# Optimization experiments

Hardware: AMD Instinct MI355X
Metric: run time of the kernel (lower is better)

Reference implementation:

```python
import jax, jax.numpy as jnp
import numpy as np

B, N, IN_CH = 4, 8192, 4
K = 16
W0, W1, W2 = 64, 128, 256
NUM_CLASSES = 3


def setup_inputs() -> dict:
    key = jax.random.key(0)
    ks = jax.random.split(key, 16)

    def lin(kw, kb, fan_in, fan_out):
        bound = 1.0 / np.sqrt(fan_in)
        w = jax.random.uniform(kw, (fan_in, fan_out), jnp.float32, -bound, bound)
        b = jax.random.uniform(kb, (fan_out,), jnp.float32, -bound, bound)
        return w, b

    x = jax.random.normal(ks[0], (B, N, IN_CH), jnp.float32)
    stem_w, stem_b = lin(ks[1], ks[2], IN_CH, W0)
    b1_w, b1_b = lin(ks[3], ks[4], 2 * W0 + 3, W1)
    b2_w, b2_b = lin(ks[5], ks[6], 2 * W1 + 3, W2)
    glob_w, glob_b = lin(ks[7], ks[8], W2, W2)
    head1_w, head1_b = lin(ks[9], ks[10], 2 * W2, W2)
    head2_w, head2_b = lin(ks[11], ks[12], W2, NUM_CLASSES)
    return {
        'x': x,
        'hmix_a': jnp.float32(1.0), 'hmix_b': jnp.float32(1.0), 'hmix_c': jnp.float32(0.0),
        'stem_w': stem_w, 'stem_b': stem_b,
        'b1_w': b1_w, 'b1_b': b1_b,
        'b2_w': b2_w, 'b2_b': b2_b,
        'glob_w': glob_w, 'glob_b': glob_b,
        'head1_w': head1_w, 'head1_b': head1_b,
        'head2_w': head2_w, 'head2_b': head2_b,
        'thresh': jnp.float32(0.15), 'sharp': jnp.float32(10.0), 'scale': jnp.float32(0.5),
    }


def _knn_idx(coords, k):
    # coords: [B,N,3] -> idx of k nearest neighbors (incl. self), no grad.
    c = jax.lax.stop_gradient(coords)
    xx = jnp.sum(c * c, axis=-1, keepdims=True)            # [B,N,1]
    dist = xx + jnp.swapaxes(xx, 1, 2) - 2.0 * jnp.einsum('bnc,bmc->bnm', c, c)
    dist = jnp.maximum(dist, 0.0)
    _, idx = jax.lax.top_k(-dist, k)                       # smallest distances
    return idx                                             # [B,N,k]


def _local_agg(coords, feat, idx, w, b):
    # gather-concat-MLP-maxpool, faithful to LocalAggBlock (pool='max')
    bidx = jnp.arange(coords.shape[0])[:, None, None]
    nb_f = feat[bidx, idx]                                 # [B,N,k,C]
    nb_p = coords[bidx, idx]                               # [B,N,k,3]
    fi = feat[:, :, None, :]
    pi = coords[:, :, None, :]
    h = jnp.concatenate(
        [jnp.broadcast_to(fi, nb_f.shape), nb_f - fi, nb_p - pi], axis=-1)
    h = jax.nn.relu(jnp.einsum('bnkd,do->bnko', h, w) + b)
    return jnp.max(h, axis=2)                              # [B,N,out]


def reference(x, hmix_a, hmix_b, hmix_c, stem_w, stem_b, b1_w, b1_b,
              b2_w, b2_b, glob_w, glob_b, head1_w, head1_b,
              head2_w, head2_b, thresh, sharp, scale):
    # HeightMixer: z_eff = a*z + b*hag + c
    z_eff = hmix_a * x[..., 2] + hmix_b * x[..., 3] + hmix_c
    coords = jnp.stack([x[..., 0], x[..., 1], z_eff], axis=-1)  # [B,N,3]

    f = jax.nn.relu(x @ stem_w + stem_b)                   # stem: [B,N,64]

    # both blocks use the same coords -> same KNN graph; compute once
    idx = _knn_idx(coords, K)
    f = _local_agg(coords, f, idx, b1_w, b1_b)             # [B,N,128]
    f = _local_agg(coords, f, idx, b2_w, b2_b)             # [B,N,256]

    g = jnp.max(f, axis=1)                                 # [B,256]
    g = jax.nn.relu(g @ glob_w + glob_b)
    g = jnp.broadcast_to(g[:, None, :], f.shape)           # [B,N,256]

    h = jnp.concatenate([f, g], axis=-1)                   # [B,N,512]
    h = jax.nn.relu(h @ head1_w + head1_b)
    logits = h @ head2_w + head2_b                         # [B,N,3]

    # HeightPriorBias on class 0
    hag = x[..., 3]
    bias = scale * jax.nn.sigmoid(sharp * (thresh - hag))
    logits = logits.at[..., 0].add(bias)
    return logits
```

## Files before the change

kernel.cpp:

```cpp
#include <hip/hip_runtime.h>
#include <math.h>

typedef unsigned long long u64;
typedef unsigned int u32;
typedef _Float16 h8v __attribute__((ext_vector_type(8)));
typedef float    f4v __attribute__((ext_vector_type(4)));
typedef float    f2v __attribute__((ext_vector_type(2)));

#define MFMA16(a,b,c) __builtin_amdgcn_mfma_f32_16x16x32_f16(a, b, c, 0, 0, 0)

#define B_ 4
#define N_ 8192
#define K_ 16
#define W0_ 64
#define W1_ 128
#define W2_ 256
#define X0_ 96
#define X1_ 160

__global__ __launch_bounds__(256) void prep_kernel(
    const float* __restrict__ x,
    const float* __restrict__ stem_w, const float* __restrict__ stem_b,
    const float* __restrict__ hmix_a, const float* __restrict__ hmix_b,
    const float* __restrict__ hmix_c,
    float* __restrict__ coords4, _Float16* __restrict__ fx0,
    _Float16* __restrict__ fx1,
    const float* __restrict__ b1_w, const float* __restrict__ b2_w,
    const float* __restrict__ h1w,
    _Float16* __restrict__ w1m, _Float16* __restrict__ w1d,
    _Float16* __restrict__ w2m, _Float16* __restrict__ w2d,
    _Float16* __restrict__ h1wT) {
  const int bi = blockIdx.x;
  const int tid = threadIdx.x;
  const int PB = (B_*N_)/4;
  if (bi < PB) {
    const int p = bi * 4 + (tid >> 6);
    const int o = tid & 63;
    const float x0 = x[p*4+0], x1 = x[p*4+1], x2 = x[p*4+2], x3 = x[p*4+3];
    const float z = hmix_a[0]*x2 + hmix_b[0]*x3 + hmix_c[0];
    float acc = stem_b[o] + x0*stem_w[0*W0_+o] + x1*stem_w[1*W0_+o]
              + x2*stem_w[2*W0_+o] + x3*stem_w[3*W0_+o];
    fx0[p*X0_+o] = (_Float16)fmaxf(acc, 0.f);
    if (o < 32) {
      const float tv = (o==0) ? x0 : (o==1) ? x1 : (o==2) ? z : 0.f;
      fx0[p*X0_+W0_+o] = (_Float16)tv;
      fx1[(size_t)p*X1_+W1_+o] = (_Float16)tv;
    }
    if (o == 0) {
      const float xx = x0*x0 + x1*x1 + z*z;
      ((float4*)coords4)[p] = make_float4(x0, x1, z, xx);
    }
  } else if (bi < PB + W1_) {
    const int o = bi - PB, c = tid;
    if (c < X0_) {
      float mv = 0.f, dv = 0.f;
      if (c < W0_)        { const float wm = b1_w[(W0_+c)*W1_+o]; mv = wm; dv = b1_w[c*W1_+o] - wm; }
      else if (c < W0_+3) { const float wp = b1_w[(2*W0_+(c-W0_))*W1_+o]; mv = wp; dv = -wp; }
      w1m[o*X0_+c] = (_Float16)mv;
      w1d[o*X0_+c] = (_Float16)dv;
    }
  } else if (bi < PB + W1_ + W2_) {
    const int o = bi - PB - W1_, c = tid;
    if (c < X1_) {
      float mv = 0.f, dv = 0.f;
      if (c < W1_)        { const float wm = b2_w[(W1_+c)*W2_+o]; mv = wm; dv = b2_w[c*W2_+o] - wm; }
      else if (c < W1_+3) { const float wp = b2_w[(2*W1_+(c-W1_))*W2_+o]; mv = wp; dv = -wp; }
      w2m[o*X1_+c] = (_Float16)mv;
      w2d[o*X1_+c] = (_Float16)dv;
    }
  } else {
    const int o = bi - PB - W1_ - W2_;
    for (int c = tid; c < 512; c += 256)
      h1wT[(size_t)o*512 + c] = (_Float16)h1w[(size_t)c*256 + o];
  }
}

#define DPP_SHR1(v) __builtin_amdgcn_update_dpp(0, (v), 0x138, 0xF, 0xF, false)

#define DPP_MIN(v, ctrl)                                                        \
  { const int _t = __builtin_amdgcn_update_dpp(__float_as_int(v),               \
      __float_as_int(v), ctrl, 0xF, 0xF, false);                                \
    v = fminf(v, __int_as_float(_t)); }

__device__ __forceinline__ float sixteenth_of_minima(float v) {
  float th = 0.f;
#pragma unroll
  for (int r = 0; r < 16; ++r) {
    float w = v;
    DPP_MIN(w, 0x111); DPP_MIN(w, 0x112); DPP_MIN(w, 0x114); DPP_MIN(w, 0x118);
    DPP_MIN(w, 0x142); DPP_MIN(w, 0x143);
    const float mv = __int_as_float(
        __builtin_amdgcn_readlane(__float_as_int(w), 63));
    th = mv;
    v = (v == mv) ? INFINITY : v;
  }
  return th;
}

#define KNN_EVT(d, dk, ik)                                                      \
  {                                                                             \
    const int s = (int)__ffsll((unsigned long long)m) - 1;  m &= m - 1;         \
    const float dc = __int_as_float(__builtin_amdgcn_readlane(                  \
                       __float_as_int(d), s));                                  \
    const bool cnd = dc < dk;                                                   \
    const u64 cm = __ballot(cnd) << 1;                                          \
    const float pd = __int_as_float(DPP_SHR1(__float_as_int(dk)));              \
    const int   pi = DPP_SHR1(ik);                                              \
    const bool pc = (cm >> lane) & 1;                                           \
    dk = cnd ? (pc ? pd : dc) : dk;                                             \
    ik = cnd ? (pc ? pi : (jbase + s)) : ik;                                    \
  }

#define KNN_CHUNK(d, dk, ik, T, Th)                                             \
  { u64 m = __ballot(d <= T);                                                   \
    if (m) {                                                                    \
      do { KNN_EVT(d, dk, ik) } while (m);                                      \
      T = fminf(Th, __int_as_float(__builtin_amdgcn_readlane(                   \
            __float_as_int(dk), 15)));                                          \
    }                                                                           \
  }

#define KNN_DIST2(dA, dB)                                                       \
  const f2v cjx = {cj.x, cj.x}, cjy = {cj.y, cj.y},                             \
            cjz = {cj.z, cj.z}, cjw = {cj.w, cj.w};                             \
  f2v tA = cAx * cjx;                                                           \
  tA = __builtin_elementwise_fma(cAy, cjy, tA);                                 \
  tA = __builtin_elementwise_fma(cAz, cjz, tA);                                 \
  const f2v dA = __builtin_elementwise_fma(tA, m2, cAw + cjw);                  \
  f2v tB = cBx * cjx;                                                           \
  tB = __builtin_elementwise_fma(cBy, cjy, tB);                                 \
  tB = __builtin_elementwise_fma(cBz, cjz, tB);                                 \
  const f2v dB = __builtin_elementwise_fma(tB, m2, cBw + cjw);

__global__ __launch_bounds__(256, 8) void knn_kernel(
    const float* __restrict__ coords4, int* __restrict__ knn_idx) {
  const int tid = threadIdx.x;
  const int wid = tid >> 6;
  const int lane = tid & 63;
  const int p0 = blockIdx.x * 16 + wid * 4;
  const int b = p0 >> 13;
  const float4* cb = ((const float4*)coords4) + (b << 13);
  const float4 c0 = ((const float4*)coords4)[p0+0];
  const float4 c1 = ((const float4*)coords4)[p0+1];
  const float4 c2 = ((const float4*)coords4)[p0+2];
  const float4 c3 = ((const float4*)coords4)[p0+3];
  const f2v m2 = {-2.f, -2.f};
  const f2v cAx = {c0.x, c1.x}, cAy = {c0.y, c1.y}, cAz = {c0.z, c1.z}, cAw = {c0.w, c1.w};
  const f2v cBx = {c2.x, c3.x}, cBy = {c2.y, c3.y}, cBz = {c2.z, c3.z}, cBw = {c2.w, c3.w};

  float lm0 = INFINITY, lm1 = INFINITY, lm2 = INFINITY, lm3 = INFINITY;
  for (int it = 0; it < 64; ++it) {
    const float4 cj = cb[it*64 + lane];
    KNN_DIST2(dA, dB)
    lm0 = fminf(lm0, fmaxf(dA[0], 0.f));
    lm1 = fminf(lm1, fmaxf(dA[1], 0.f));
    lm2 = fminf(lm2, fmaxf(dB[0], 0.f));
    lm3 = fminf(lm3, fmaxf(dB[1], 0.f));
  }
  const float Th0 = sixteenth_of_minima(lm0);
  const float Th1 = sixteenth_of_minima(lm1);
  const float Th2 = sixteenth_of_minima(lm2);
  const float Th3 = sixteenth_of_minima(lm3);

  float dk0 = INFINITY, dk1 = INFINITY, dk2 = INFINITY, dk3 = INFINITY;
  int   ik0 = 0, ik1 = 0, ik2 = 0, ik3 = 0;
  float T0 = Th0, T1 = Th1, T2 = Th2, T3 = Th3;

  for (int it = 0; it < N_/64; ++it) {
    const int jbase = it*64;
    const float4 cj = cb[jbase + lane];
    KNN_DIST2(dA, dB)
    const float d0 = fmaxf(dA[0], 0.f);
    const float d1 = fmaxf(dA[1], 0.f);
    const float d2 = fmaxf(dB[0], 0.f);
    const float d3 = fmaxf(dB[1], 0.f);
    KNN_CHUNK(d0, dk0, ik0, T0, Th0);
    KNN_CHUNK(d1, dk1, ik1, T1, Th1);
    KNN_CHUNK(d2, dk2, ik2, T2, Th2);
    KNN_CHUNK(d3, dk3, ik3, T3, Th3);
  }

  if (lane < K_) {
    knn_idx[(size_t)(p0+0)*K_ + lane] = ik0;
    knn_idx[(size_t)(p0+1)*K_ + lane] = ik1;
    knn_idx[(size_t)(p0+2)*K_ + lane] = ik2;
    knn_idx[(size_t)(p0+3)*K_ + lane] = ik3;
  }
}

template<int KS, int NPASS, bool GMAX>
__global__ __launch_bounds__(256) void aggm_kernel(
    const _Float16* __restrict__ fx, const int* __restrict__ knn_idx,
    const _Float16* __restrict__ midT, const _Float16* __restrict__ difT,
    const float* __restrict__ bw,
    _Float16* __restrict__ fo, const int ostr, u32* __restrict__ part) {
  const int XD  = KS*32;
  const int XDP = XD + 8;
  const int CH  = KS*4;
  const int p0 = blockIdx.x * 16;
  const int bb = (p0 >> 13) << 13;
  const int tid = threadIdx.x;
  const int w = tid >> 6, lane = tid & 63, col = lane & 15, quad = lane >> 4;
  const int koff = quad * 8;

  __shared__ int s_idx[256];
  __shared__ _Float16 sA[2][16*(KS*32+8)];

  s_idx[tid] = knn_idx[p0*K_ + tid];

  f4v cacc[NPASS][2];
  {
    h8v Ao[KS];
    const _Float16* ap = fx + (size_t)(p0+col)*XD + koff;
#pragma unroll
    for (int kk = 0; kk < KS; ++kk) Ao[kk] = *(const h8v*)(ap + kk*32);
#pragma unroll
    for (int ps = 0; ps < NPASS; ++ps) {
      const int o0 = ps*128 + w*32;
      const _Float16* b0 = difT + (size_t)(o0 + col)*XD + koff;
      const _Float16* b1 = difT + (size_t)(o0 + 16 + col)*XD + koff;
      f4v c0 = {0.f,0.f,0.f,0.f}, c1 = {0.f,0.f,0.f,0.f};
#pragma unroll
      for (int kk = 0; kk < KS; ++kk) {
        c0 = MFMA16(Ao[kk], *(const h8v*)(b0 + kk*32), c0);
        c1 = MFMA16(Ao[kk], *(const h8v*)(b1 + kk*32), c1);
      }
      cacc[ps][0] = c0; cacc[ps][1] = c1;
    }
  }

  h8v Bf[NPASS][2][KS];
  float bias[NPASS][2];
#pragma unroll
  for (int ps = 0; ps < NPASS; ++ps) {
    const int o0 = ps*128 + w*32;
#pragma unroll
    for (int kk = 0; kk < KS; ++kk) {
      Bf[ps][0][kk] = *(const h8v*)(midT + (size_t)(o0 + col)*XD + kk*32 + koff);
      Bf[ps][1][kk] = *(const h8v*)(midT + (size_t)(o0 + 16 + col)*XD + kk*32 + koff);
    }
    bias[ps][0] = bw[o0 + col];
    bias[ps][1] = bw[o0 + 16 + col];
  }
  __syncthreads();

  for (int c = tid; c < 16*CH; c += 256) {
    const int r = c / CH, o = c - r*CH;
    *(uint4*)&sA[0][r*XDP + o*8] =
        *(const uint4*)(fx + (size_t)(bb + s_idx[r<<4])*XD + o*8);
  }
  __syncthreads();

  f4v M[NPASS][2];
#pragma unroll
  for (int ps = 0; ps < NPASS; ++ps) {
    M[ps][0] = (f4v){-INFINITY,-INFINITY,-INFINITY,-INFINITY};
    M[ps][1] = (f4v){-INFINITY,-INFINITY,-INFINITY,-INFINITY};
  }

  for (int k = 0; k < 16; ++k) {
    const int buf = k & 1;
    if (k < 15) {
      for (int c = tid; c < 16*CH; c += 256) {
        const int r = c / CH, o = c - r*CH;
        *(uint4*)&sA[buf^1][r*XDP + o*8] =
            *(const uint4*)(fx + (size_t)(bb + s_idx[(r<<4) + k + 1])*XD + o*8);
      }
    }
    h8v Ac[KS];
    const _Float16* ap = &sA[buf][col*XDP + koff];
#pragma unroll
    for (int kk = 0; kk < KS; ++kk) Ac[kk] = *(const h8v*)(ap + kk*32);
#pragma unroll
    for (int ps = 0; ps < NPASS; ++ps) {
      f4v d0 = {0.f,0.f,0.f,0.f}, d1 = {0.f,0.f,0.f,0.f};
#pragma unroll
      for (int kk = 0; kk < KS; ++kk) {
        d0 = MFMA16(Ac[kk], Bf[ps][0][kk], d0);
        d1 = MFMA16(Ac[kk], Bf[ps][1][kk], d1);
      }
#pragma unroll
      for (int e = 0; e < 4; ++e) {
        M[ps][0][e] = fmaxf(M[ps][0][e], d0[e]);
        M[ps][1][e] = fmaxf(M[ps][1][e], d1[e]);
      }
    }
    __syncthreads();
  }

  const int prow = p0 + (quad << 2);
  const int bq = p0 >> 13;
#pragma unroll
  for (int ps = 0; ps < NPASS; ++ps) {
    const int o0 = ps*128 + w*32;
    const int oa = o0 + col, ob = oa + 16;
    float v0[4], v1[4];
#pragma unroll
    for (int reg = 0; reg < 4; ++reg) {
      v0[reg] = fmaxf(M[ps][0][reg] + cacc[ps][0][reg] + bias[ps][0], 0.f);
      v1[reg] = fmaxf(M[ps][1][reg] + cacc[ps][1][reg] + bias[ps][1], 0.f);
      fo[(size_t)(prow+reg)*ostr + oa] = (_Float16)v0[reg];
      fo[(size_t)(prow+reg)*ostr + ob] = (_Float16)v1[reg];
    }
    if (GMAX) {
      float bm0 = fmaxf(fmaxf(v0[0], v0[1]), fmaxf(v0[2], v0[3]));
      float bm1 = fmaxf(fmaxf(v1[0], v1[1]), fmaxf(v1[2], v1[3]));
      bm0 = fmaxf(bm0, __shfl_xor(bm0, 16, 64));
      bm0 = fmaxf(bm0, __shfl_xor(bm0, 32, 64));
      bm1 = fmaxf(bm1, __shfl_xor(bm1, 16, 64));
      bm1 = fmaxf(bm1, __shfl_xor(bm1, 32, 64));
      if (quad == 0) {
        atomicMax(part + bq*W2_ + oa, __float_as_uint(bm0));
        atomicMax(part + bq*W2_ + ob, __float_as_uint(bm1));
      }
    }
  }
}

__global__ __launch_bounds__(256) void gfc_kernel(
    const float* __restrict__ part, const float* __restrict__ gw,
    const float* __restrict__ gb, _Float16* __restrict__ g2h) {
  const int b = blockIdx.x;
  const int o = threadIdx.x;
  __shared__ float s_g[W2_];
  s_g[o] = part[b*W2_ + o];
  __syncthreads();
  float acc = gb[o];
  for (int d = 0; d < W2_; ++d) acc += s_g[d]*gw[d*W2_ + o];
  g2h[b*W2_ + o] = (_Float16)fmaxf(acc, 0.f);
}

__global__ __launch_bounds__(256) void headm_kernel(
    const _Float16* __restrict__ f2h, const _Float16* __restrict__ g2h,
    const _Float16* __restrict__ h1wT, const float* __restrict__ h1b,
    const float* __restrict__ h2w, const float* __restrict__ h2b,
    const float* __restrict__ x,
    const float* __restrict__ thresh, const float* __restrict__ sharp,
    const float* __restrict__ scale,
    float* __restrict__ out) {
  const int p0 = blockIdx.x * 32;
  const int b = p0 >> 13;
  const int tid = threadIdx.x;
  const int w = tid >> 6, lane = tid & 63, col = lane & 15, quad = lane >> 4;

  __shared__ _Float16 sA[32*520];
  __shared__ float    sh[32*260];

  for (int t = tid; t < 32*32; t += 256) {
    const int r = t >> 5, cc = (t & 31) * 8;
    *(uint4*)&sA[r*520 + cc] = *(const uint4*)&f2h[(size_t)(p0+r)*W2_ + cc];
  }
  for (int t = tid; t < 32*32; t += 256) {
    const int r = t >> 5, cc = (t & 31) * 8;
    *(uint4*)&sA[r*520 + 256 + cc] = *(const uint4*)&g2h[b*W2_ + cc];
  }
  __syncthreads();

  f4v acc[2][4];
#pragma unroll
  for (int r = 0; r < 2; ++r)
#pragma unroll
    for (int t = 0; t < 4; ++t) acc[r][t] = (f4v){0.f,0.f,0.f,0.f};

  for (int kk = 0; kk < 16; ++kk) {
    const h8v a0 = *(const h8v*)&sA[col*520 + kk*32 + quad*8];
    const h8v a1 = *(const h8v*)&sA[(16+col)*520 + kk*32 + quad*8];
#pragma unroll
    for (int t = 0; t < 4; ++t) {
      const h8v bt = *(const h8v*)&h1wT[(size_t)(w*64 + t*16 + col)*512 + kk*32 + quad*8];
      acc[0][t] = MFMA16(a0, bt, acc[0][t]);
      acc[1][t] = MFMA16(a1, bt, acc[1][t]);
    }
  }
#pragma unroll
  for (int r = 0; r < 2; ++r)
#pragma unroll
    for (int t = 0; t < 4; ++t) {
      const int o = w*64 + t*16 + col;
      const float bv = h1b[o];
#pragma unroll
      for (int reg = 0; reg < 4; ++reg)
        sh[(r*16 + quad*4 + reg)*260 + o] = fmaxf(acc[r][t][reg] + bv, 0.f);
    }
  __syncthreads();

  if (tid < 96) {
    const int pp = tid / 3, c = tid % 3;
    float s = h2b[c];
    for (int d = 0; d < 256; ++d) s += sh[pp*260 + d] * h2w[d*3 + c];
    if (c == 0) {
      const float hag = x[(size_t)(p0+pp)*4 + 3];
      s += scale[0] / (1.f + expf(-sharp[0]*(thresh[0] - hag)));
    }
    out[(size_t)(p0+pp)*3 + c] = s;
  }
}

extern "C" void kernel_launch(void* const* d_in, const int* in_sizes, int n_in,
                              void* d_out, int out_size, void* d_ws, size_t ws_size,
                              hipStream_t stream) {
  const float* x       = (const float*)d_in[0];
  const float* hmix_a  = (const float*)d_in[1];
  const float* hmix_b  = (const float*)d_in[2];
  const float* hmix_c  = (const float*)d_in[3];
  const float* stem_w  = (const float*)d_in[4];
  const float* stem_b  = (const float*)d_in[5];
  const float* b1_w    = (const float*)d_in[6];
  const float* b1_b    = (const float*)d_in[7];
  const float* b2_w    = (const float*)d_in[8];
  const float* b2_b    = (const float*)d_in[9];
  const float* glob_w  = (const float*)d_in[10];
  const float* glob_b  = (const float*)d_in[11];
  const float* head1_w = (const float*)d_in[12];
  const float* head1_b = (const float*)d_in[13];
  const float* head2_w = (const float*)d_in[14];
  const float* head2_b = (const float*)d_in[15];
  const float* thresh  = (const float*)d_in[16];
  const float* sharp   = (const float*)d_in[17];
  const float* scale   = (const float*)d_in[18];
  float* out = (float*)d_out;

  char* base = (char*)d_ws;
  float*     coords4 = (float*)    (base + 0);
  int*       idxb    = (int*)      (base + 524288);
  _Float16*  fx0     = (_Float16*) (base + 2621440);
  _Float16*  fx1     = (_Float16*) (base + 8912896);
  _Float16*  f2h     = (_Float16*) (base + 19398656);
  _Float16*  w1m     = (_Float16*) (base + 36175872);
  _Float16*  w1d     = (_Float16*) (base + 36200448);
  _Float16*  w2m     = (_Float16*) (base + 36225024);
  _Float16*  w2d     = (_Float16*) (base + 36306944);
  _Float16*  h1wT    = (_Float16*) (base + 36388864);
  float*     part    = (float*)    (base + 36651008);
  _Float16*  g2h     = (_Float16*) (base + 36782080);

  const int NP = B_ * N_;

  prep_kernel<<<NP/4 + W1_ + 2*W2_, 256, 0, stream>>>(
      x, stem_w, stem_b, hmix_a, hmix_b, hmix_c, coords4, fx0, fx1,
      b1_w, b2_w, head1_w, w1m, w1d, w2m, w2d, h1wT);
  hipMemsetAsync(part, 0, B_*W2_*sizeof(float), stream);
  knn_kernel<<<NP/16, 256, 0, stream>>>(coords4, idxb);
  aggm_kernel<3, 1, false><<<NP/16, 256, 0, stream>>>(
      fx0, idxb, w1m, w1d, b1_b, fx1, X1_, (u32*)0);
  aggm_kernel<5, 2, true><<<NP/16, 256, 0, stream>>>(
      fx1, idxb, w2m, w2d, b2_b, f2h, W2_, (u32*)part);
  gfc_kernel<<<B_, 256, 0, stream>>>(part, glob_w, glob_b, g2h);
  headm_kernel<<<NP/32, 256, 0, stream>>>(f2h, g2h, h1wT, head1_b, head2_w, head2_b,
                                          x, thresh, sharp, scale, out);
}
```

Measured before the change: 445.1 us.

## Widen KNN to 8 queries per wave, fold memset and global FC into neighbors

The KNN kernel now processes 8 query points per wave instead of 4, so each loaded candidate coordinate is reused across more distance computations, and the occupancy hint is dropped. The memset of the pooled-max buffer moves into an extra prep block. The global FC kernel is removed and recomputed redundantly in every head block, with the g half of the A operand read directly from shared memory. This trims launches and shared memory but adds per-block redundant 256x256 FC work and higher register pressure in KNN with half as many blocks.

```diff
diff --git a/kernel.cpp b/kernel.cpp
--- a/kernel.cpp
+++ b/kernel.cpp
@@ -29,7 +29,7 @@
     const float* __restrict__ h1w,
     _Float16* __restrict__ w1m, _Float16* __restrict__ w1d,
     _Float16* __restrict__ w2m, _Float16* __restrict__ w2d,
-    _Float16* __restrict__ h1wT) {
+    _Float16* __restrict__ h1wT, float* __restrict__ part) {
   const int bi = blockIdx.x;
   const int tid = threadIdx.x;
   const int PB = (B_*N_)/4;
@@ -68,10 +68,12 @@
       w2m[o*X1_+c] = (_Float16)mv;
       w2d[o*X1_+c] = (_Float16)dv;
     }
-  } else {
+  } else if (bi < PB + W1_ + 2*W2_) {
     const int o = bi - PB - W1_ - W2_;
     for (int c = tid; c < 512; c += 256)
       h1wT[(size_t)o*512 + c] = (_Float16)h1w[(size_t)c*256 + o];
+  } else {
+    ((float4*)part)[tid] = make_float4(0.f, 0.f, 0.f, 0.f);
   }
 }
 
@@ -120,71 +122,76 @@
     }                                                                           \
   }
 
-#define KNN_DIST2(dA, dB)                                                       \
+#define KNN_DIST8                                                               \
   const f2v cjx = {cj.x, cj.x}, cjy = {cj.y, cj.y},                             \
             cjz = {cj.z, cj.z}, cjw = {cj.w, cj.w};                             \
-  f2v tA = cAx * cjx;                                                           \
-  tA = __builtin_elementwise_fma(cAy, cjy, tA);                                 \
-  tA = __builtin_elementwise_fma(cAz, cjz, tA);                                 \
-  const f2v dA = __builtin_elementwise_fma(tA, m2, cAw + cjw);                  \
-  f2v tB = cBx * cjx;                                                           \
-  tB = __builtin_elementwise_fma(cBy, cjy, tB);                                 \
-  tB = __builtin_elementwise_fma(cBz, cjz, tB);                                 \
-  const f2v dB = __builtin_elementwise_fma(tB, m2, cBw + cjw);
-
-__global__ __launch_bounds__(256, 8) void knn_kernel(
+  f2v dd[4];                                                                    \
+  _Pragma("unroll")                                                             \
+  for (int q = 0; q < 4; ++q) {                                                 \
+    f2v t = cx[q] * cjx;                                                        \
+    t = __builtin_elementwise_fma(cy[q], cjy, t);                               \
+    t = __builtin_elementwise_fma(cz[q], cjz, t);                               \
+    const f2v dr = __builtin_elementwise_fma(t, m2, cw[q] + cjw);               \
+    dd[q] = __builtin_elementwise_max(dr, (f2v){0.f, 0.f});                     \
+  }
+
+__global__ __launch_bounds__(256) void knn_kernel(
     const float* __restrict__ coords4, int* __restrict__ knn_idx) {
   const int tid = threadIdx.x;
   const int wid = tid >> 6;
   const int lane = tid & 63;
-  const int p0 = blockIdx.x * 16 + wid * 4;
+  const int p0 = blockIdx.x * 32 + wid * 8;
   const int b = p0 >> 13;
   const float4* cb = ((const float4*)coords4) + (b << 13);
-  const float4 c0 = ((const float4*)coords4)[p0+0];
-  const float4 c1 = ((const float4*)coords4)[p0+1];
-  const float4 c2 = ((const float4*)coords4)[p0+2];
-  const float4 c3 = ((const float4*)coords4)[p0+3];
   const f2v m2 = {-2.f, -2.f};
-  const f2v cAx = {c0.x, c1.x}, cAy = {c0.y, c1.y}, cAz = {c0.z, c1.z}, cAw = {c0.w, c1.w};
-  const f2v cBx = {c2.x, c3.x}, cBy = {c2.y, c3.y}, cBz = {c2.z, c3.z}, cBw = {c2.w, c3.w};
-
-  float lm0 = INFINITY, lm1 = INFINITY, lm2 = INFINITY, lm3 = INFINITY;
+
+  f2v cx[4], cy[4], cz[4], cw[4];
+#pragma unroll
+  for (int q = 0; q < 4; ++q) {
+    const float4 ca = ((const float4*)coords4)[p0 + 2*q];
+    const float4 cbq = ((const float4*)coords4)[p0 + 2*q + 1];
+    cx[q] = (f2v){ca.x, cbq.x}; cy[q] = (f2v){ca.y, cbq.y};
+    cz[q] = (f2v){ca.z, cbq.z}; cw[q] = (f2v){ca.w, cbq.w};
+  }
+
+  float lm[8];
+#pragma unroll
+  for (int i = 0; i < 8; ++i) lm[i] = INFINITY;
   for (int it = 0; it < 64; ++it) {
     const float4 cj = cb[it*64 + lane];
-    KNN_DIST2(dA, dB)
-    lm0 = fminf(lm0, fmaxf(dA[0], 0.f));
-    lm1 = fminf(lm1, fmaxf(dA[1], 0.f));
-    lm2 = fminf(lm2, fmaxf(dB[0], 0.f));
-    lm3 = fminf(lm3, fmaxf(dB[1], 0.f));
-  }
-  const float Th0 = sixteenth_of_minima(lm0);
-  const float Th1 = sixteenth_of_minima(lm1);
-  const float Th2 = sixteenth_of_minima(lm2);
-  const float Th3 = sixteenth_of_minima(lm3);
-
-  float dk0 = INFINITY, dk1 = INFINITY, dk2 = INFINITY, dk3 = INFINITY;
-  int   ik0 = 0, ik1 = 0, ik2 = 0, ik3 = 0;
-  float T0 = Th0, T1 = Th1, T2 = Th2, T3 = Th3;
+    KNN_DIST8
+#pragma unroll
+    for (int i = 0; i < 8; ++i) lm[i] = fminf(lm[i], dd[i>>1][i&1]);
+  }
+
+  float Th[8], T[8], dk[8];
+  int ik[8];
+#pragma unroll
+  for (int i = 0; i < 8; ++i) {
+    Th[i] = sixteenth_of_minima(lm[i]);
+    T[i] = Th[i];
+    dk[i] = INFINITY;
+    ik[i] = 0;
+  }
 
   for (int it = 0; it < N_/64; ++it) {
     const int jbase = it*64;
     const float4 cj = cb[jbase + lane];
-    KNN_DIST2(dA, dB)
-    const float d0 = fmaxf(dA[0], 0.f);
-    const float d1 = fmaxf(dA[1], 0.f);
-    const float d2 = fmaxf(dB[0], 0.f);
-    const float d3 = fmaxf(dB[1], 0.f);
-    KNN_CHUNK(d0, dk0, ik0, T0, Th0);
-    KNN_CHUNK(d1, dk1, ik1, T1, Th1);
-    KNN_CHUNK(d2, dk2, ik2, T2, Th2);
-    KNN_CHUNK(d3, dk3, ik3, T3, Th3);
+    KNN_DIST8
+    KNN_CHUNK(dd[0][0], dk[0], ik[0], T[0], Th[0]);
+    KNN_CHUNK(dd[0][1], dk[1], ik[1], T[1], Th[1]);
+    KNN_CHUNK(dd[1][0], dk[2], ik[2], T[2], Th[2]);
+    KNN_CHUNK(dd[1][1], dk[3], ik[3], T[3], Th[3]);
+    KNN_CHUNK(dd[2][0], dk[4], ik[4], T[4], Th[4]);
+    KNN_CHUNK(dd[2][1], dk[5], ik[5], T[5], Th[5]);
+    KNN_CHUNK(dd[3][0], dk[6], ik[6], T[6], Th[6]);
+    KNN_CHUNK(dd[3][1], dk[7], ik[7], T[7], Th[7]);
   }
 
   if (lane < K_) {
-    knn_idx[(size_t)(p0+0)*K_ + lane] = ik0;
-    knn_idx[(size_t)(p0+1)*K_ + lane] = ik1;
-    knn_idx[(size_t)(p0+2)*K_ + lane] = ik2;
-    knn_idx[(size_t)(p0+3)*K_ + lane] = ik3;
+#pragma unroll
+    for (int i = 0; i < 8; ++i)
+      knn_idx[(size_t)(p0+i)*K_ + lane] = ik[i];
   }
 }
 
@@ -317,21 +324,9 @@
   }
 }
 
-__global__ __launch_bounds__(256) void gfc_kernel(
-    const float* __restrict__ part, const float* __restrict__ gw,
-    const float* __restrict__ gb, _Float16* __restrict__ g2h) {
-  const int b = blockIdx.x;
-  const int o = threadIdx.x;
-  __shared__ float s_g[W2_];
-  s_g[o] = part[b*W2_ + o];
-  __syncthreads();
-  float acc = gb[o];
-  for (int d = 0; d < W2_; ++d) acc += s_g[d]*gw[d*W2_ + o];
-  g2h[b*W2_ + o] = (_Float16)fmaxf(acc, 0.f);
-}
-
 __global__ __launch_bounds__(256) void headm_kernel(
-    const _Float16* __restrict__ f2h, const _Float16* __restrict__ g2h,
+    const _Float16* __restrict__ f2h, const float* __restrict__ part,
+    const float* __restrict__ gw, const float* __restrict__ gb,
     const _Float16* __restrict__ h1wT, const float* __restrict__ h1b,
     const float* __restrict__ h2w, const float* __restrict__ h2b,
     const float* __restrict__ x,
@@ -343,28 +338,41 @@
   const int tid = threadIdx.x;
   const int w = tid >> 6, lane = tid & 63, col = lane & 15, quad = lane >> 4;
 
-  __shared__ _Float16 sA[32*520];
+  __shared__ float    s_part[W2_];
+  __shared__ _Float16 s_gh[W2_];
+  __shared__ _Float16 sA[32*264];
   __shared__ float    sh[32*260];
 
+  s_part[tid] = part[b*W2_ + tid];
   for (int t = tid; t < 32*32; t += 256) {
     const int r = t >> 5, cc = (t & 31) * 8;
-    *(uint4*)&sA[r*520 + cc] = *(const uint4*)&f2h[(size_t)(p0+r)*W2_ + cc];
-  }
-  for (int t = tid; t < 32*32; t += 256) {
-    const int r = t >> 5, cc = (t & 31) * 8;
-    *(uint4*)&sA[r*520 + 256 + cc] = *(const uint4*)&g2h[b*W2_ + cc];
+    *(uint4*)&sA[r*264 + cc] = *(const uint4*)&f2h[(size_t)(p0+r)*W2_ + cc];
   }
   __syncthreads();
 
+  {
+    float gacc = gb[tid];
+    for (int d = 0; d < W2_; ++d) gacc += s_part[d]*gw[d*W2_ + tid];
+    s_gh[tid] = (_Float16)fmaxf(gacc, 0.f);
+  }
+  __syncthreads();
+
   f4v acc[2][4];
 #pragma unroll
   for (int r = 0; r < 2; ++r)
 #pragma unroll
     for (int t = 0; t < 4; ++t) acc[r][t] = (f4v){0.f,0.f,0.f,0.f};
 
+#pragma unroll
   for (int kk = 0; kk < 16; ++kk) {
-    const h8v a0 = *(const h8v*)&sA[col*520 + kk*32 + quad*8];
-    const h8v a1 = *(const h8v*)&sA[(16+col)*520 + kk*32 + quad*8];
+    h8v a0, a1;
+    if (kk < 8) {
+      a0 = *(const h8v*)&sA[col*264 + kk*32 + quad*8];
+      a1 = *(const h8v*)&sA[(16+col)*264 + kk*32 + quad*8];
+    } else {
+      a0 = *(const h8v*)&s_gh[(kk-8)*32 + quad*8];
+      a1 = a0;
+    }
 #pragma unroll
     for (int t = 0; t < 4; ++t) {
       const h8v bt = *(const h8v*)&h1wT[(size_t)(w*64 + t*16 + col)*512 + kk*32 + quad*8];
@@ -432,20 +440,17 @@
   _Float16*  w2d     = (_Float16*) (base + 36306944);
   _Float16*  h1wT    = (_Float16*) (base + 36388864);
   float*     part    = (float*)    (base + 36651008);
-  _Float16*  g2h     = (_Float16*) (base + 36782080);
-
   const int NP = B_ * N_;
 
-  prep_kernel<<<NP/4 + W1_ + 2*W2_, 256, 0, stream>>>(
+  prep_kernel<<<NP/4 + W1_ + 2*W2_ + 1, 256, 0, stream>>>(
       x, stem_w, stem_b, hmix_a, hmix_b, hmix_c, coords4, fx0, fx1,
-      b1_w, b2_w, head1_w, w1m, w1d, w2m, w2d, h1wT);
-  hipMemsetAsync(part, 0, B_*W2_*sizeof(float), stream);
-  knn_kernel<<<NP/16, 256, 0, stream>>>(coords4, idxb);
+      b1_w, b2_w, head1_w, w1m, w1d, w2m, w2d, h1wT, part);
+  knn_kernel<<<NP/32, 256, 0, stream>>>(coords4, idxb);
   aggm_kernel<3, 1, false><<<NP/16, 256, 0, stream>>>(
       fx0, idxb, w1m, w1d, b1_b, fx1, X1_, (u32*)0);
   aggm_kernel<5, 2, true><<<NP/16, 256, 0, stream>>>(
       fx1, idxb, w2m, w2d, b2_b, f2h, W2_, (u32*)part);
-  gfc_kernel<<<B_, 256, 0, stream>>>(part, glob_w, glob_b, g2h);
-  headm_kernel<<<NP/32, 256, 0, stream>>>(f2h, g2h, h1wT, head1_b, head2_w, head2_b,
+  headm_kernel<<<NP/32, 256, 0, stream>>>(f2h, part, glob_w, glob_b,
+                                          h1wT, head1_b, head2_w, head2_b,
                                           x, thresh, sharp, scale, out);
 }
```

Result: slower. 457.6 us (+2.8%).
